# Kernel tuning notes

Hardware: AMD Instinct MI355X
Metric: run time of the kernel (lower is better)

## Reference

```python
import jax, jax.numpy as jnp
import numpy as np

B, T, D = 4, 1024, 256
H, DK, C = 8, 32, 16  # n_heads, d_key, pos-encoder hidden units
DV = D // H
NEG = -1e15
EPS_SM = 1e-5
EPS_LN = 1e-5
SLOPE = 0.01  # LeakyReLU default


def setup_inputs() -> dict:
    key = jax.random.key(0)
    ks = jax.random.split(key, 16)
    s = 0.05
    x = jax.random.normal(ks[0], (B, T, D), jnp.float32)
    src_mask = jax.random.randint(ks[1], (B, T, T), 0, 2).astype(bool)
    rel_dists = jax.random.uniform(ks[2], (B, 1, T, T), jnp.float32)
    Wq = jax.random.normal(ks[3], (H, DK, D), jnp.float32) * s
    Wk = jax.random.normal(ks[4], (H, DK, D), jnp.float32) * s
    Wv = jax.random.normal(ks[5], (H, DV, D), jnp.float32) * s
    pw1 = jax.random.normal(ks[6], (H, C), jnp.float32) * s
    pb1 = jax.random.normal(ks[7], (H, C), jnp.float32) * s
    pw2 = jax.random.normal(ks[8], (H, C), jnp.float32) * s
    pb2 = jax.random.normal(ks[9], (H,), jnp.float32) * s
    Wo = jax.random.normal(ks[10], (D, D), jnp.float32) * s
    bo = jax.random.normal(ks[11], (D,), jnp.float32) * s
    Wf = jax.random.normal(ks[12], (D, D), jnp.float32) * s
    bf = jax.random.normal(ks[13], (D,), jnp.float32) * s
    g1 = jnp.ones((D,), jnp.float32)
    beta1 = jnp.zeros((D,), jnp.float32)
    g2 = jnp.ones((D,), jnp.float32)
    beta2 = jnp.zeros((D,), jnp.float32)
    return dict(x=x, src_mask=src_mask, rel_dists=rel_dists, Wq=Wq, Wk=Wk, Wv=Wv,
                pw1=pw1, pb1=pb1, pw2=pw2, pb2=pb2, Wo=Wo, bo=bo, Wf=Wf, bf=bf,
                g1=g1, beta1=beta1, g2=g2, beta2=beta2)


def _l2norm(v):
    # F.normalize(p=2, dim=-1): v / max(||v||, 1e-12)
    n = jnp.sqrt(jnp.sum(v * v, axis=-1, keepdims=True))
    return v / jnp.maximum(n, 1e-12)


def _lrelu(h):
    return jnp.where(h >= 0, h, SLOPE * h)


def _pos_bias(d, pw1, pb1, pw2, pb2):
    # d: [B,T,T]; per-head 1x1-conv MLP applied elementwise.
    # Loop over the tiny channel dim (16) to avoid a [B,H,T,T,C] intermediate.
    bias = jnp.broadcast_to(pb2[None, :, None, None], (d.shape[0], pw1.shape[0], d.shape[1], d.shape[2]))
    for c in range(pw1.shape[1]):
        h = d[:, None] * pw1[None, :, c, None, None] + pb1[None, :, c, None, None]
        bias = bias + pw2[None, :, c, None, None] * _lrelu(h)
    return bias  # [B,H,T,T]


def _layer_norm(v, g, b):
    mu = jnp.mean(v, axis=-1, keepdims=True)
    var = jnp.mean((v - mu) ** 2, axis=-1, keepdims=True)
    return (v - mu) * jax.lax.rsqrt(var + EPS_LN) * g + b


def reference(x, src_mask, rel_dists, Wq, Wk, Wv, pw1, pb1, pw2, pb2,
              Wo, bo, Wf, bf, g1, beta1, g2, beta2):
    # cosine-normalized multi-head attention (all heads batched)
    q = _l2norm(jnp.einsum('btd,hkd->bhtk', x, Wq))
    k = _l2norm(jnp.einsum('bsd,hkd->bhsk', x, Wk))
    v = jnp.einsum('bsd,hvd->bhsv', x, Wv)
    logits = jnp.einsum('bhtk,bhsk->bhts', q, k)
    logits = logits - _pos_bias(rel_dists[:, 0], pw1, pb1, pw2, pb2)
    logits = jnp.where(src_mask[:, None], NEG, logits)
    # custom softmax: exp / (sum + 1e-5) (handles all-padded rows)
    z = jnp.exp(logits)
    attn = z / (jnp.sum(z, axis=-1, keepdims=True) + EPS_SM)
    heads = jnp.einsum('bhts,bhsv->bhtv', attn, v)
    y = heads.transpose(0, 2, 1, 3).reshape(x.shape[0], x.shape[1], -1)  # concat heads
    y = y @ Wo.T + bo
    # residual + LN + FFN (dropout is identity in eval mode)
    zz = _layer_norm(x + y, g1, beta1)
    z_ff = _lrelu(zz @ Wf.T + bf)
    return _layer_norm(zz + z_ff, g2, beta2)
```

## Files before the change

### kernel.cpp

```cpp
#include <hip/hip_runtime.h>
#include <math.h>

#define Tc 1024
#define Dc 256
#define Hc 8
#define Cc 16
#define LUTN 256

typedef __attribute__((ext_vector_type(8))) short short8;
typedef __attribute__((ext_vector_type(4))) float f32x4;

__device__ __forceinline__ unsigned bf16u(float x) {
    unsigned u = __float_as_uint(x);
    return (u + 0x7FFFu + ((u >> 16) & 1u)) >> 16;
}
__device__ __forceinline__ unsigned pk2(float lo, float hi) {
    return bf16u(lo) | (bf16u(hi) << 16);
}
__device__ __forceinline__ unsigned pk2t(float lo, float hi) {
    return __builtin_amdgcn_perm(__float_as_uint(hi), __float_as_uint(lo), 0x07060302u);
}
__device__ __forceinline__ float upk(unsigned v) { return __uint_as_float(v << 16); }
__device__ __forceinline__ float upkh(unsigned v) { return __uint_as_float(v & 0xffff0000u); }

__device__ __forceinline__ short8 packW8(const float* __restrict__ p) {
    float4 b0 = *(const float4*)(p);
    float4 b1 = *(const float4*)(p + 4);
    union { short8 s; unsigned wds[4]; } B;
    B.wds[0] = pk2(b0.x, b0.y); B.wds[1] = pk2(b0.z, b0.w);
    B.wds[2] = pk2(b1.x, b1.y); B.wds[3] = pk2(b1.z, b1.w);
    return B.s;
}

__global__ __launch_bounds__(256) void qkv_direct(
    const float* __restrict__ x,
    const float* __restrict__ Wq, const float* __restrict__ Wk,
    const float* __restrict__ Wv,
    ushort* __restrict__ Qb, ushort* __restrict__ Kb, ushort* __restrict__ Vt)
{
    const int tid = threadIdx.x;
    const int w = tid >> 6;
    const int l = tid & 63;
    const int u = l & 15, g = l >> 4;
    const int rbase = blockIdx.x * 16;
    const int cb = (blockIdx.y * 4 + w) * 64;
    const int mat = cb >> 8;
    const int fcb = cb & 255;
    const float* Wmat = (mat == 0) ? Wq : (mat == 1) ? Wk : Wv;

    f32x4 acc[4];
#pragma unroll
    for (int nt = 0; nt < 4; ++nt) acc[nt] = (f32x4){0.f, 0.f, 0.f, 0.f};

    const float* arow = x + (size_t)(rbase + u) * 256 + g * 8;
#pragma unroll 2
    for (int k0 = 0; k0 < 256; k0 += 32) {
        short8 af = packW8(arow + k0);
#pragma unroll
        for (int nt = 0; nt < 4; ++nt) {
            short8 bfr = packW8(Wmat + (size_t)(fcb + nt * 16 + u) * 256 + k0 + g * 8);
            acc[nt] = __builtin_amdgcn_mfma_f32_16x16x32_bf16(af, bfr, acc[nt], 0, 0, 0);
        }
    }

    if (mat < 2) {
        ushort* Out = (mat == 0) ? Qb : Kb;
#pragma unroll
        for (int hp = 0; hp < 2; ++hp) {
            const int head = (fcb >> 5) + hp;
#pragma unroll
            for (int reg = 0; reg < 4; ++reg) {
                float ss = acc[2 * hp][reg] * acc[2 * hp][reg]
                         + acc[2 * hp + 1][reg] * acc[2 * hp + 1][reg];
                ss += __shfl_xor(ss, 1, 64);
                ss += __shfl_xor(ss, 2, 64);
                ss += __shfl_xor(ss, 4, 64);
                ss += __shfl_xor(ss, 8, 64);
                float scn = 1.f / fmaxf(sqrtf(ss), 1e-12f);
                const int t = rbase + 4 * g + reg;
                const int bb = t >> 10, tt = t & 1023;
                const size_t base = ((size_t)(bb * 8 + head) * Tc + tt) * 32;
                Out[base + u]      = (ushort)bf16u(acc[2 * hp][reg] * scn);
                Out[base + 16 + u] = (ushort)bf16u(acc[2 * hp + 1][reg] * scn);
            }
        }
    } else {
#pragma unroll
        for (int nt = 0; nt < 4; ++nt) {
            const int head = (fcb >> 5) + (nt >> 1);
            const int vt = nt & 1;
#pragma unroll
            for (int reg = 0; reg < 4; ++reg) {
                const int s = rbase + 4 * g + reg;
                const int bb = s >> 10, ss = s & 1023;
                const int bh = bb * 8 + head;
                Vt[(((size_t)bh * 32 + (ss >> 5)) * 2 + vt) * 512 + u * 32 + (ss & 31)] =
                    (ushort)bf16u(acc[nt][reg]);
            }
        }
    }
}

__global__ __launch_bounds__(256) void attn_mfma(
    const ushort* __restrict__ Qb, const ushort* __restrict__ Kb,
    const ushort* __restrict__ Vt,
    const float* __restrict__ rel, const int* __restrict__ msk,
    const float* __restrict__ pw1, const float* __restrict__ pb1,
    const float* __restrict__ pw2, const float* __restrict__ pb2,
    ushort* __restrict__ Yb)
{
    const int tid = threadIdx.x;
    const int w = tid >> 6;
    const int l = tid & 63;
    const int u = l & 15;
    const int g = l >> 4;
    const int t0 = blockIdx.x * 16;
    const int b = blockIdx.y;
    const int hg = blockIdx.z;

    __shared__ __align__(16) ushort lut_s[1024];
    __shared__ __align__(16) ushort comb[4 * 16 * 72];
    __shared__ float rs_s[8 * 16];

    {
        const int bin = tid;
        const float d0 = bin * (1.f / LUTN), d1 = (bin + 1) * (1.f / LUTN);
#pragma unroll
        for (int hp = 0; hp < 2; ++hp) {
            const int h = hg * 2 + hp;
            float y0 = pb2[h], y1 = pb2[h];
#pragma unroll
            for (int c = 0; c < Cc; ++c) {
                float w1 = pw1[h * Cc + c], b1 = pb1[h * Cc + c], w2 = pw2[h * Cc + c];
                float h0 = fmaf(w1, d0, b1), h1 = fmaf(w1, d1, b1);
                y0 = fmaf(w2, h0 >= 0.f ? h0 : 0.01f * h0, y0);
                y1 = fmaf(w2, h1 >= 0.f ? h1 : 0.01f * h1, y1);
            }
            float a = (y1 - y0) * (float)LUTN;
            float bq = y0 - a * d0;
            lut_s[bin * 4 + hp * 2]     = (ushort)bf16u(a);
            lut_s[bin * 4 + hp * 2 + 1] = (ushort)bf16u(bq);
        }
    }

    const int bh0 = b * 8 + hg * 2;
    short8 qf[2];
#pragma unroll
    for (int hi = 0; hi < 2; ++hi)
        qf[hi] = *(const short8*)(Qb + (((size_t)(bh0 + hi) * Tc + t0 + u) * 32 + g * 8));

    const short8 ones = (short8){0x3F80, 0x3F80, 0x3F80, 0x3F80,
                                 0x3F80, 0x3F80, 0x3F80, 0x3F80};

    f32x4 oacc[2][2];
    f32x4 rsacc[2];
#pragma unroll
    for (int hi = 0; hi < 2; ++hi) {
        oacc[hi][0] = (f32x4){0.f, 0.f, 0.f, 0.f};
        oacc[hi][1] = (f32x4){0.f, 0.f, 0.f, 0.f};
        rsacc[hi]   = (f32x4){0.f, 0.f, 0.f, 0.f};
    }

    __syncthreads();

    const int s_begin = w * 256;
    const float* rrow = rel + (size_t)b * Tc * Tc + (size_t)(t0 + u) * Tc;
    const int*   mrow = msk + (size_t)b * Tc * Tc + (size_t)(t0 + u) * Tc;

    float4 r0c = *(const float4*)(rrow + s_begin + 8 * g);
    float4 r1c = *(const float4*)(rrow + s_begin + 8 * g + 4);
    int4   m0c = *(const int4*)(mrow + s_begin + 8 * g);
    int4   m1c = *(const int4*)(mrow + s_begin + 8 * g + 4);
    short8 kc[2][2];
#pragma unroll
    for (int hi = 0; hi < 2; ++hi) {
        const size_t kb = ((size_t)(bh0 + hi) * Tc + s_begin + 2 * u) * 32 + g * 8;
        kc[hi][0] = *(const short8*)(Kb + kb);
        kc[hi][1] = *(const short8*)(Kb + kb + 32);
    }

    for (int sc = s_begin; sc < s_begin + 256; sc += 32) {
        const int nx = (sc + 32 < s_begin + 256) ? sc + 32 : s_begin;
        float4 r0n = *(const float4*)(rrow + nx + 8 * g);
        float4 r1n = *(const float4*)(rrow + nx + 8 * g + 4);
        int4   m0n = *(const int4*)(mrow + nx + 8 * g);
        int4   m1n = *(const int4*)(mrow + nx + 8 * g + 4);
        short8 kn[2][2];
#pragma unroll
        for (int hi = 0; hi < 2; ++hi) {
            const size_t kb = ((size_t)(bh0 + hi) * Tc + nx + 2 * u) * 32 + g * 8;
            kn[hi][0] = *(const short8*)(Kb + kb);
            kn[hi][1] = *(const short8*)(Kb + kb + 32);
        }

        const float rv[8] = {r0c.x, r0c.y, r0c.z, r0c.w, r1c.x, r1c.y, r1c.z, r1c.w};
        const int   mv[8] = {m0c.x, m0c.y, m0c.z, m0c.w, m1c.x, m1c.y, m1c.z, m1c.w};
        float dA[4], dB[4];
#pragma unroll
        for (int j = 0; j < 4; ++j) {
            dA[j] = mv[2 * j]     ? -1.f : rv[2 * j];
            dB[j] = mv[2 * j + 1] ? -1.f : rv[2 * j + 1];
        }
        float biasA[4][2], biasB[4][2];
#pragma unroll
        for (int j = 0; j < 4; ++j) {
            int iA = (int)(dA[j] * (float)LUTN);
            int iB = (int)(dB[j] * (float)LUTN);
            iA = iA < 0 ? 0 : (iA > LUTN - 1 ? LUTN - 1 : iA);
            iB = iB < 0 ? 0 : (iB > LUTN - 1 ? LUTN - 1 : iB);
            uint2 wA = *(const uint2*)(lut_s + iA * 4);
            uint2 wB = *(const uint2*)(lut_s + iB * 4);
            biasA[j][0] = fmaf(upk(wA.x), dA[j], upkh(wA.x));
            biasA[j][1] = fmaf(upk(wA.y), dA[j], upkh(wA.y));
            biasB[j][0] = fmaf(upk(wB.x), dB[j], upkh(wB.x));
            biasB[j][1] = fmaf(upk(wB.y), dB[j], upkh(wB.y));
        }
#pragma unroll
        for (int hi = 0; hi < 2; ++hi) {
            const f32x4 z4 = (f32x4){0.f, 0.f, 0.f, 0.f};
            f32x4 sA = __builtin_amdgcn_mfma_f32_16x16x32_bf16(kc[hi][0], qf[hi], z4, 0, 0, 0);
            f32x4 sB = __builtin_amdgcn_mfma_f32_16x16x32_bf16(kc[hi][1], qf[hi], z4, 0, 0, 0);
            union { short8 s; unsigned w4[4]; } P;
#pragma unroll
            for (int j = 0; j < 4; ++j) {
                float zA = (dA[j] < 0.f) ? 0.f : __expf(sA[j] - biasA[j][hi]);
                float zB = (dB[j] < 0.f) ? 0.f : __expf(sB[j] - biasB[j][hi]);
                P.w4[j] = pk2t(zA, zB);
            }
            const ushort* vb = Vt + ((size_t)(bh0 + hi) * 32 + (sc >> 5)) * 1024;
            short8 vf0 = *(const short8*)(vb + u * 32 + g * 8);
            short8 vf1 = *(const short8*)(vb + 512 + u * 32 + g * 8);
            oacc[hi][0] = __builtin_amdgcn_mfma_f32_16x16x32_bf16(P.s, vf0, oacc[hi][0], 0, 0, 0);
            oacc[hi][1] = __builtin_amdgcn_mfma_f32_16x16x32_bf16(P.s, vf1, oacc[hi][1], 0, 0, 0);
            rsacc[hi]   = __builtin_amdgcn_mfma_f32_16x16x32_bf16(P.s, ones, rsacc[hi], 0, 0, 0);
        }
        r0c = r0n; r1c = r1n; m0c = m0n; m1c = m1n;
#pragma unroll
        for (int hi = 0; hi < 2; ++hi) {
            kc[hi][0] = kn[hi][0];
            kc[hi][1] = kn[hi][1];
        }
    }

#pragma unroll
    for (int hi = 0; hi < 2; ++hi)
        if (u == 0) {
#pragma unroll
            for (int reg = 0; reg < 4; ++reg)
                rs_s[(w * 2 + hi) * 16 + 4 * g + reg] = rsacc[hi][reg];
        }
#pragma unroll
    for (int hi = 0; hi < 2; ++hi)
#pragma unroll
        for (int vt = 0; vt < 2; ++vt)
#pragma unroll
            for (int reg = 0; reg < 4; ++reg)
                comb[w * 1152 + (4 * g + reg) * 72 + hi * 32 + vt * 16 + u] =
                    (ushort)(__float_as_uint(oacc[hi][vt][reg]) >> 16);
    __syncthreads();

    if (tid < 128) {
        const int tl = tid >> 3;
        const int f0 = (tid & 7) * 8;
        const int hl = f0 >> 5;
        float rstot = rs_s[hl * 16 + tl] + rs_s[(2 + hl) * 16 + tl]
                    + rs_s[(4 + hl) * 16 + tl] + rs_s[(6 + hl) * 16 + tl];
        float inv = 1.f / (rstot + 1e-5f);
        float o[8];
#pragma unroll
        for (int k = 0; k < 8; ++k) o[k] = 0.f;
#pragma unroll
        for (int ww = 0; ww < 4; ++ww) {
            uint4 pv = *(const uint4*)&comb[ww * 1152 + tl * 72 + f0];
            o[0] += upk(pv.x); o[1] += upkh(pv.x);
            o[2] += upk(pv.y); o[3] += upkh(pv.y);
            o[4] += upk(pv.z); o[5] += upkh(pv.z);
            o[6] += upk(pv.w); o[7] += upkh(pv.w);
        }
        uint4 pwv;
        pwv.x = pk2(o[0] * inv, o[1] * inv); pwv.y = pk2(o[2] * inv, o[3] * inv);
        pwv.z = pk2(o[4] * inv, o[5] * inv); pwv.w = pk2(o[6] * inv, o[7] * inv);
        *(uint4*)(Yb + ((size_t)b * Tc + t0 + tl) * Dc + hg * 64 + f0) = pwv;
    }
}

__global__ __launch_bounds__(512) void out_fused(
    const ushort* __restrict__ Yb, const float* __restrict__ Wo,
    const float* __restrict__ bo, const float* __restrict__ x,
    const float* __restrict__ g1, const float* __restrict__ be1,
    const float* __restrict__ Wf, const float* __restrict__ bfb,
    const float* __restrict__ g2, const float* __restrict__ be2,
    float* __restrict__ out)
{
    const int tid = threadIdx.x;
    const int w = tid >> 6;
    const int l = tid & 63;
    const int u = l & 15, g = l >> 4;
    const int rbase = blockIdx.x * 16;

    __shared__ float red1[128], red2[128];
    __shared__ __align__(16) ushort ZZs[16 * 256];

    f32x4 acc[2];
    acc[0] = (f32x4){0.f, 0.f, 0.f, 0.f};
    acc[1] = (f32x4){0.f, 0.f, 0.f, 0.f};
    const ushort* arow = Yb + (size_t)(rbase + u) * 256 + g * 8;
#pragma unroll 2
    for (int k0 = 0; k0 < 256; k0 += 32) {
        short8 af = *(const short8*)(arow + k0);
#pragma unroll
        for (int nt = 0; nt < 2; ++nt) {
            short8 bfr = packW8(Wo + (size_t)(w * 32 + nt * 16 + u) * 256 + k0 + g * 8);
            acc[nt] = __builtin_amdgcn_mfma_f32_16x16x32_bf16(af, bfr, acc[nt], 0, 0, 0);
        }
    }

    float bv[2];
#pragma unroll
    for (int nt = 0; nt < 2; ++nt) bv[nt] = bo[w * 32 + nt * 16 + u];

    float sv[4][2];
#pragma unroll
    for (int reg = 0; reg < 4; ++reg) {
        const int row = rbase + 4 * g + reg;
        float s1 = 0.f, s2 = 0.f;
#pragma unroll
        for (int nt = 0; nt < 2; ++nt) {
            const int col = w * 32 + nt * 16 + u;
            float s = acc[nt][reg] + bv[nt] + x[(size_t)row * 256 + col];
            sv[reg][nt] = s;
            s1 += s;
            s2 = fmaf(s, s, s2);
        }
        s1 += __shfl_xor(s1, 1, 64); s2 += __shfl_xor(s2, 1, 64);
        s1 += __shfl_xor(s1, 2, 64); s2 += __shfl_xor(s2, 2, 64);
        s1 += __shfl_xor(s1, 4, 64); s2 += __shfl_xor(s2, 4, 64);
        s1 += __shfl_xor(s1, 8, 64); s2 += __shfl_xor(s2, 8, 64);
        if (u == 0) { red1[w * 16 + 4 * g + reg] = s1; red2[w * 16 + 4 * g + reg] = s2; }
    }
    __syncthreads();

    float zzv[4][2];
#pragma unroll
    for (int reg = 0; reg < 4; ++reg) {
        const int rl = 4 * g + reg;
        float S1 = 0.f, S2 = 0.f;
#pragma unroll
        for (int ww = 0; ww < 8; ++ww) { S1 += red1[ww * 16 + rl]; S2 += red2[ww * 16 + rl]; }
        float mu = S1 * (1.f / 256.f);
        float var = S2 * (1.f / 256.f) - mu * mu;
        float rsig = rsqrtf(var + 1e-5f);
#pragma unroll
        for (int nt = 0; nt < 2; ++nt) {
            const int col = w * 32 + nt * 16 + u;
            float zz = (sv[reg][nt] - mu) * rsig * g1[col] + be1[col];
            zzv[reg][nt] = zz;
            const int boff = (rl * 512 + col * 2) ^ ((rl & 7) << 4);
            *(ushort*)((char*)ZZs + boff) = (ushort)bf16u(zz);
        }
    }
    __syncthreads();

    f32x4 acc2[2];
    acc2[0] = (f32x4){0.f, 0.f, 0.f, 0.f};
    acc2[1] = (f32x4){0.f, 0.f, 0.f, 0.f};
#pragma unroll 2
    for (int k0 = 0; k0 < 256; k0 += 32) {
        const int aoff = (u * 512 + (k0 + g * 8) * 2) ^ ((u & 7) << 4);
        short8 af = *(const short8*)((const char*)ZZs + aoff);
#pragma unroll
        for (int nt = 0; nt < 2; ++nt) {
            short8 bfr = packW8(Wf + (size_t)(w * 32 + nt * 16 + u) * 256 + k0 + g * 8);
            acc2[nt] = __builtin_amdgcn_mfma_f32_16x16x32_bf16(af, bfr, acc2[nt], 0, 0, 0);
        }
    }

    float bv2[2];
#pragma unroll
    for (int nt = 0; nt < 2; ++nt) bv2[nt] = bfb[w * 32 + nt * 16 + u];

    float sv2[4][2];
#pragma unroll
    for (int reg = 0; reg < 4; ++reg) {
        float s1 = 0.f, s2 = 0.f;
#pragma unroll
        for (int nt = 0; nt < 2; ++nt) {
            float v = acc2[nt][reg] + bv2[nt];
            v = v >= 0.f ? v : 0.01f * v;
            float s = v + zzv[reg][nt];
            sv2[reg][nt] = s;
            s1 += s;
            s2 = fmaf(s, s, s2);
        }
        s1 += __shfl_xor(s1, 1, 64); s2 += __shfl_xor(s2, 1, 64);
        s1 += __shfl_xor(s1, 2, 64); s2 += __shfl_xor(s2, 2, 64);
        s1 += __shfl_xor(s1, 4, 64); s2 += __shfl_xor(s2, 4, 64);
        s1 += __shfl_xor(s1, 8, 64); s2 += __shfl_xor(s2, 8, 64);
        if (u == 0) { red1[w * 16 + 4 * g + reg] = s1; red2[w * 16 + 4 * g + reg] = s2; }
    }
    __syncthreads();

#pragma unroll
    for (int reg = 0; reg < 4; ++reg) {
        const int row = rbase + 4 * g + reg;
        const int rl = 4 * g + reg;
        float S1 = 0.f, S2 = 0.f;
#pragma unroll
        for (int ww = 0; ww < 8; ++ww) { S1 += red1[ww * 16 + rl]; S2 += red2[ww * 16 + rl]; }
        float mu = S1 * (1.f / 256.f);
        float var = S2 * (1.f / 256.f) - mu * mu;
        float rsig = rsqrtf(var + 1e-5f);
#pragma unroll
        for (int nt = 0; nt < 2; ++nt) {
            const int col = w * 32 + nt * 16 + u;
            out[(size_t)row * 256 + col] = (sv2[reg][nt] - mu) * rsig * g2[col] + be2[col];
        }
    }
}

extern "C" void kernel_launch(void* const* d_in, const int* in_sizes, int n_in,
                              void* d_out, int out_size, void* d_ws, size_t ws_size,
                              hipStream_t stream) {
    const float* x    = (const float*)d_in[0];
    const int*   mask = (const int*)d_in[1];
    const float* rel  = (const float*)d_in[2];
    const float* Wq   = (const float*)d_in[3];
    const float* Wk   = (const float*)d_in[4];
    const float* Wv   = (const float*)d_in[5];
    const float* pw1  = (const float*)d_in[6];
    const float* pb1  = (const float*)d_in[7];
    const float* pw2  = (const float*)d_in[8];
    const float* pb2  = (const float*)d_in[9];
    const float* Wo   = (const float*)d_in[10];
    const float* bo   = (const float*)d_in[11];
    const float* Wf   = (const float*)d_in[12];
    const float* bf   = (const float*)d_in[13];
    const float* g1   = (const float*)d_in[14];
    const float* be1  = (const float*)d_in[15];
    const float* g2   = (const float*)d_in[16];
    const float* be2  = (const float*)d_in[17];
    float* out = (float*)d_out;

    char* wsb = (char*)d_ws;
    ushort* Qb = (ushort*)(wsb);
    ushort* Kb = (ushort*)(wsb + (size_t)(2 << 20));
    ushort* Vt = (ushort*)(wsb + (size_t)(4 << 20));
    ushort* Yb = (ushort*)(wsb + (size_t)(6 << 20));

    qkv_direct<<<dim3(256, 3), 256, 0, stream>>>(x, Wq, Wk, Wv, Qb, Kb, Vt);
    attn_mfma<<<dim3(64, 4, 4), 256, 0, stream>>>(Qb, Kb, Vt, rel, mask,
                                                  pw1, pb1, pw2, pb2, Yb);
    out_fused<<<256, 512, 0, stream>>>(Yb, Wo, bo, x, g1, be1,
                                       Wf, bf, g2, be2, out);
}
```

Baseline: 201.2 us.

## Prepack rel_dists and mask into bf16 buffer and swizzle attention grid for reuse

Adds a pre-pass kernel that merges the float distance matrix and the int mask into one bf16 array, using -1 as the masked sentinel. The attention kernel then reads one 2-byte value per element instead of 8 bytes. The grid is flattened and remapped so the four head-group blocks sharing a (batch, row-tile) run close together, which should help them reuse the packed data from cache. The cost is an extra kernel launch and pass over the inputs, plus bf16 rounding of the distances before the LUT lookup.

```diff
diff --git a/kernel.cpp b/kernel.cpp
--- a/kernel.cpp
+++ b/kernel.cpp
@@ -30,6 +30,23 @@
     B.wds[0] = pk2(b0.x, b0.y); B.wds[1] = pk2(b0.z, b0.w);
     B.wds[2] = pk2(b1.x, b1.y); B.wds[3] = pk2(b1.z, b1.w);
     return B.s;
+}
+
+__global__ __launch_bounds__(256) void pack_dm(
+    const float* __restrict__ rel, const int* __restrict__ msk,
+    ushort* __restrict__ Dm)
+{
+    const int idx = (blockIdx.x * 256 + threadIdx.x) * 8;
+    float4 d0 = *(const float4*)(rel + idx);
+    float4 d1 = *(const float4*)(rel + idx + 4);
+    int4   m0 = *(const int4*)(msk + idx);
+    int4   m1 = *(const int4*)(msk + idx + 4);
+    uint4 p;
+    p.x = (m0.x ? 0xBF80u : bf16u(d0.x)) | ((m0.y ? 0xBF80u : bf16u(d0.y)) << 16);
+    p.y = (m0.z ? 0xBF80u : bf16u(d0.z)) | ((m0.w ? 0xBF80u : bf16u(d0.w)) << 16);
+    p.z = (m1.x ? 0xBF80u : bf16u(d1.x)) | ((m1.y ? 0xBF80u : bf16u(d1.y)) << 16);
+    p.w = (m1.z ? 0xBF80u : bf16u(d1.z)) | ((m1.w ? 0xBF80u : bf16u(d1.w)) << 16);
+    *(uint4*)(Dm + idx) = p;
 }
 
 __global__ __launch_bounds__(256) void qkv_direct(
@@ -103,8 +120,7 @@
 
 __global__ __launch_bounds__(256) void attn_mfma(
     const ushort* __restrict__ Qb, const ushort* __restrict__ Kb,
-    const ushort* __restrict__ Vt,
-    const float* __restrict__ rel, const int* __restrict__ msk,
+    const ushort* __restrict__ Vt, const ushort* __restrict__ Dm,
     const float* __restrict__ pw1, const float* __restrict__ pb1,
     const float* __restrict__ pw2, const float* __restrict__ pb2,
     ushort* __restrict__ Yb)
@@ -114,9 +130,12 @@
     const int l = tid & 63;
     const int u = l & 15;
     const int g = l >> 4;
-    const int t0 = blockIdx.x * 16;
-    const int b = blockIdx.y;
-    const int hg = blockIdx.z;
+    const int bid = blockIdx.x;
+    const int c   = bid & 7;
+    const int hg  = (bid >> 3) & 3;
+    const int tb  = (bid >> 5) * 8 + c;
+    const int t0  = (tb & 63) * 16;
+    const int b   = tb >> 6;
 
     __shared__ __align__(16) ushort lut_s[1024];
     __shared__ __align__(16) ushort comb[4 * 16 * 72];
@@ -130,8 +149,8 @@
             const int h = hg * 2 + hp;
             float y0 = pb2[h], y1 = pb2[h];
 #pragma unroll
-            for (int c = 0; c < Cc; ++c) {
-                float w1 = pw1[h * Cc + c], b1 = pb1[h * Cc + c], w2 = pw2[h * Cc + c];
+            for (int cc = 0; cc < Cc; ++cc) {
+                float w1 = pw1[h * Cc + cc], b1 = pb1[h * Cc + cc], w2 = pw2[h * Cc + cc];
                 float h0 = fmaf(w1, d0, b1), h1 = fmaf(w1, d1, b1);
                 y0 = fmaf(w2, h0 >= 0.f ? h0 : 0.01f * h0, y0);
                 y1 = fmaf(w2, h1 >= 0.f ? h1 : 0.01f * h1, y1);
@@ -164,13 +183,9 @@
     __syncthreads();
 
     const int s_begin = w * 256;
-    const float* rrow = rel + (size_t)b * Tc * Tc + (size_t)(t0 + u) * Tc;
-    const int*   mrow = msk + (size_t)b * Tc * Tc + (size_t)(t0 + u) * Tc;
-
-    float4 r0c = *(const float4*)(rrow + s_begin + 8 * g);
-    float4 r1c = *(const float4*)(rrow + s_begin + 8 * g + 4);
-    int4   m0c = *(const int4*)(mrow + s_begin + 8 * g);
-    int4   m1c = *(const int4*)(mrow + s_begin + 8 * g + 4);
+    const ushort* drow = Dm + (size_t)b * Tc * Tc + (size_t)(t0 + u) * Tc;
+
+    uint4 dmv = *(const uint4*)(drow + s_begin + 8 * g);
     short8 kc[2][2];
 #pragma unroll
     for (int hi = 0; hi < 2; ++hi) {
@@ -181,10 +196,7 @@
 
     for (int sc = s_begin; sc < s_begin + 256; sc += 32) {
         const int nx = (sc + 32 < s_begin + 256) ? sc + 32 : s_begin;
-        float4 r0n = *(const float4*)(rrow + nx + 8 * g);
-        float4 r1n = *(const float4*)(rrow + nx + 8 * g + 4);
-        int4   m0n = *(const int4*)(mrow + nx + 8 * g);
-        int4   m1n = *(const int4*)(mrow + nx + 8 * g + 4);
+        uint4 dmn = *(const uint4*)(drow + nx + 8 * g);
         short8 kn[2][2];
 #pragma unroll
         for (int hi = 0; hi < 2; ++hi) {
@@ -193,13 +205,12 @@
             kn[hi][1] = *(const short8*)(Kb + kb + 32);
         }
 
-        const float rv[8] = {r0c.x, r0c.y, r0c.z, r0c.w, r1c.x, r1c.y, r1c.z, r1c.w};
-        const int   mv[8] = {m0c.x, m0c.y, m0c.z, m0c.w, m1c.x, m1c.y, m1c.z, m1c.w};
+        const unsigned dw[4] = {dmv.x, dmv.y, dmv.z, dmv.w};
         float dA[4], dB[4];
 #pragma unroll
         for (int j = 0; j < 4; ++j) {
-            dA[j] = mv[2 * j]     ? -1.f : rv[2 * j];
-            dB[j] = mv[2 * j + 1] ? -1.f : rv[2 * j + 1];
+            dA[j] = upk(dw[j]);
+            dB[j] = upkh(dw[j]);
         }
         float biasA[4][2], biasB[4][2];
 #pragma unroll
@@ -234,7 +245,7 @@
             oacc[hi][1] = __builtin_amdgcn_mfma_f32_16x16x32_bf16(P.s, vf1, oacc[hi][1], 0, 0, 0);
             rsacc[hi]   = __builtin_amdgcn_mfma_f32_16x16x32_bf16(P.s, ones, rsacc[hi], 0, 0, 0);
         }
-        r0c = r0n; r1c = r1n; m0c = m0n; m1c = m1n;
+        dmv = dmn;
 #pragma unroll
         for (int hi = 0; hi < 2; ++hi) {
             kc[hi][0] = kn[hi][0];
@@ -446,10 +457,12 @@
     ushort* Kb = (ushort*)(wsb + (size_t)(2 << 20));
     ushort* Vt = (ushort*)(wsb + (size_t)(4 << 20));
     ushort* Yb = (ushort*)(wsb + (size_t)(6 << 20));
-
+    ushort* Dm = (ushort*)(wsb + (size_t)(8 << 20));
+
+    pack_dm<<<2048, 256, 0, stream>>>(rel, mask, Dm);
     qkv_direct<<<dim3(256, 3), 256, 0, stream>>>(x, Wq, Wk, Wv, Qb, Kb, Vt);
-    attn_mfma<<<dim3(64, 4, 4), 256, 0, stream>>>(Qb, Kb, Vt, rel, mask,
-                                                  pw1, pb1, pw2, pb2, Yb);
+    attn_mfma<<<1024, 256, 0, stream>>>(Qb, Kb, Vt, Dm,
+                                        pw1, pb1, pw2, pb2, Yb);
     out_fused<<<256, 512, 0, stream>>>(Yb, Wo, bo, x, g1, be1,
                                        Wf, bf, g2, be2, out);
 }
```

Result: faster. 192.9 us (-4.2%).
